# Kernel optimization log

Hardware: AMD Instinct MI355X
Metric: run time of the kernel (lower is better)

Reference implementation:

```python
import jax, jax.numpy as jnp
import numpy as np

EPS = 1e-5

def _conv1x1(x, w, b):
    # x: [B,C,H,W], w: [O,C], b: [O]
    return jnp.einsum('bchw,oc->bohw', x, w) + b[None, :, None, None]

def setup_inputs() -> dict:
    key = jax.random.key(0)
    ks = jax.random.split(key, 6)
    B, C, H, W = 8, 512, 64, 64
    Ck, Cv, Co = 256, 256, 512
    x = jax.random.normal(ks[0], (B, C, H, W), dtype=jnp.float32)
    Wk = jax.random.normal(ks[1], (Ck, C), dtype=jnp.float32) * 0.02
    bk = jnp.zeros((Ck,), dtype=jnp.float32)
    gamma = jnp.ones((Ck,), dtype=jnp.float32)
    beta = jnp.zeros((Ck,), dtype=jnp.float32)
    Wv = jax.random.normal(ks[2], (Cv, C), dtype=jnp.float32) * 0.02
    bv = jnp.zeros((Cv,), dtype=jnp.float32)
    Ww = jax.random.normal(ks[3], (Co, Cv), dtype=jnp.float32) * 0.02
    bw = jnp.zeros((Co,), dtype=jnp.float32)
    return {'x': x, 'Wk': Wk, 'bk': bk, 'gamma': gamma, 'beta': beta,
            'Wv': Wv, 'bv': bv, 'Ww': Ww, 'bw': bw}

def reference(x, Wk, bk, gamma, beta, Wv, bv, Ww, bw):
    B, C, H, W = x.shape
    # f_key == f_query (shared module): conv1x1 -> BN (training stats) -> ReLU
    qk = _conv1x1(x, Wk, bk)                      # [B,Ck,H,W]
    mean = qk.mean(axis=(0, 2, 3))
    var = qk.var(axis=(0, 2, 3))                  # biased variance, as torch BN training
    feat = jax.nn.relu((qk - mean[None, :, None, None])
                       * jax.lax.rsqrt(var + EPS)[None, :, None, None]
                       * gamma[None, :, None, None] + beta[None, :, None, None])
    value = _conv1x1(x, Wv, bv)                   # [B,Cv,H,W]
    Ck = feat.shape[1]
    Cv = value.shape[1]
    N = H * W
    q = feat.reshape(B, Ck, N).transpose(0, 2, 1)  # [B,N,Ck]
    k = feat.reshape(B, Ck, N)                     # [B,Ck,N]
    v = value.reshape(B, Cv, N).transpose(0, 2, 1) # [B,N,Cv]
    scale = Ck ** (-0.5)
    sim = jax.nn.softmax(jnp.matmul(q, k) * scale, axis=-1)  # [B,N,N]
    ctx = jnp.matmul(sim, v)                       # [B,N,Cv]
    ctx = ctx.transpose(0, 2, 1).reshape(B, Cv, H, W)
    out = _conv1x1(ctx, Ww, bw)                    # [B,Co,H,W]
    # scale==1 -> visualize_* upsamples are identity; sim_map visual is None
    return (out, feat, feat, value)
```

## Files before the change

### kernel.cpp

```cpp
#include <hip/hip_runtime.h>
#include <math.h>

constexpr int  Bn  = 8;
constexpr int  Cin = 512;
constexpr int  Nn  = 4096;
constexpr int  Ck  = 256;
constexpr int  Cv  = 256;
constexpr int  Co  = 512;

constexpr size_t F1_OFF  = (size_t)Bn * Co * Nn;
constexpr size_t F2_OFF  = F1_OFF + (size_t)Bn * Ck * Nn;
constexpr size_t VAL_OFF = F2_OFF + (size_t)Bn * Ck * Nn;

typedef __attribute__((ext_vector_type(8)))  short  short8;
typedef __attribute__((ext_vector_type(16))) float  f32x16;
typedef __attribute__((ext_vector_type(8)))  ushort ushort8;

static __device__ __forceinline__ ushort f2bf(float f) {
    union { float f; unsigned u; } x; x.f = f;
    unsigned r = x.u + 0x7fffu + ((x.u >> 16) & 1u);
    return (ushort)(r >> 16);
}

static __device__ __forceinline__ void gll16(const void* g, void* l) {
    __builtin_amdgcn_global_load_lds(
        (const __attribute__((address_space(1))) void*)g,
        (__attribute__((address_space(3))) void*)l, 16, 0, 0);
}

__global__ __launch_bounds__(256) void cast_w(const float* __restrict__ a,
                                              const float* __restrict__ b,
                                              const float* __restrict__ c,
                                              ushort* __restrict__ da,
                                              ushort* __restrict__ db,
                                              ushort* __restrict__ dc)
{
    const int tid   = blockIdx.x * 256 + threadIdx.x;
    const int which = tid >> 14;
    const int off   = (tid & 16383) * 8;
    const float* s = (which == 0) ? a : (which == 1) ? b : c;
    ushort*      d = (which == 0) ? da : (which == 1) ? db : dc;
    const float4 u = *(const float4*)(s + off);
    const float4 v = *(const float4*)(s + off + 4);
    ushort8 o;
    o[0] = f2bf(u.x); o[1] = f2bf(u.y); o[2] = f2bf(u.z); o[3] = f2bf(u.w);
    o[4] = f2bf(v.x); o[5] = f2bf(v.y); o[6] = f2bf(v.z); o[7] = f2bf(v.w);
    *(ushort8*)(d + off) = o;
}

__global__ __launch_bounds__(256) void transpose_c(const float* __restrict__ src,
                                                   ushort* __restrict__ dst, int C)
{
    const int b  = blockIdx.z;
    const int c0 = blockIdx.y * 64;
    const int n0 = blockIdx.x * 64;
    const int t  = threadIdx.x;
    __shared__ float T[64][65];
#pragma unroll
    for (int p = 0; p < 16; ++p) {
        const int flat = p * 256 + t;
        const int cc = flat >> 6, nn = flat & 63;
        T[cc][nn] = src[((size_t)b * C + c0 + cc) * Nn + n0 + nn];
    }
    __syncthreads();
#pragma unroll
    for (int p = 0; p < 16; ++p) {
        const int flat = p * 256 + t;
        const int nn = flat >> 6, cc = flat & 63;
        dst[((size_t)b * Nn + n0 + nn) * C + c0 + cc] = f2bf(T[cc][nn]);
    }
}

template <int K, bool DUAL>
__global__ __launch_bounds__(256) void gemm_bf(const ushort* __restrict__ XT,
                                               const ushort* __restrict__ Wb,
                                               const float*  __restrict__ bias,
                                               float* __restrict__ out,
                                               ushort* __restrict__ out_bf,
                                               int M)
{
    const int b  = blockIdx.z;
    const int m0 = blockIdx.y * 128;
    const int n0 = blockIdx.x * 128;
    const int t  = threadIdx.x;
    const int w  = t >> 6, L = t & 63;
    const int l31 = L & 31, hl = L >> 5;
    const int wm = (w >> 1) * 64, wn = (w & 1) * 64;

    __shared__ __align__(16) short As[128][72];
    __shared__ __align__(16) short Bs[128][72];

    const ushort* Xb = XT + (size_t)b * Nn * K;

    f32x16 acc[2][2];
#pragma unroll
    for (int a = 0; a < 2; ++a)
#pragma unroll
        for (int bb = 0; bb < 2; ++bb)
#pragma unroll
            for (int r = 0; r < 16; ++r) acc[a][bb][r] = 0.f;

    for (int k0 = 0; k0 < K; k0 += 64) {
        __syncthreads();
#pragma unroll
        for (int p = 0; p < 4; ++p) {
            const int e   = p * 256 + t;
            const int row = e >> 3, ko = (e & 7) * 8;
            *(short8*)&As[row][ko] =
                *(const short8*)(Wb + (size_t)(m0 + row) * K + k0 + ko);
            *(short8*)&Bs[row][ko] =
                *(const short8*)(Xb + (size_t)(n0 + row) * K + k0 + ko);
        }
        __syncthreads();
#pragma unroll
        for (int kc = 0; kc < 4; ++kc) {
            short8 Af[2], Bf[2];
#pragma unroll
            for (int a = 0; a < 2; ++a)
                Af[a] = *(const short8*)&As[wm + a * 32 + l31][kc * 16 + hl * 8];
#pragma unroll
            for (int bb = 0; bb < 2; ++bb)
                Bf[bb] = *(const short8*)&Bs[wn + bb * 32 + l31][kc * 16 + hl * 8];
#pragma unroll
            for (int a = 0; a < 2; ++a)
#pragma unroll
                for (int bb = 0; bb < 2; ++bb)
                    acc[a][bb] = __builtin_amdgcn_mfma_f32_32x32x16_bf16(
                        Af[a], Bf[bb], acc[a][bb], 0, 0, 0);
        }
    }

#pragma unroll
    for (int a = 0; a < 2; ++a)
#pragma unroll
        for (int r = 0; r < 16; ++r) {
            const int row = (r & 3) + 8 * (r >> 2) + 4 * hl;
            const int o   = m0 + wm + a * 32 + row;
            const float bv = bias[o];
            const size_t base = ((size_t)b * M + o) * Nn + n0 + wn + l31;
#pragma unroll
            for (int bb = 0; bb < 2; ++bb) {
                const float vv = acc[a][bb][r] + bv;
                out[base + bb * 32] = vv;
                if (DUAL) out_bf[base + bb * 32] = f2bf(vv);
            }
        }
}

__global__ __launch_bounds__(256) void bn_stats(const float* __restrict__ qk,
                                                const float* __restrict__ gamma,
                                                const float* __restrict__ beta,
                                                float* __restrict__ ss)
{
    const int o = blockIdx.x;
    const int t = threadIdx.x;
    float s = 0.f, sq = 0.f;
    for (int b = 0; b < Bn; ++b) {
        const float* p = qk + ((size_t)b * Ck + o) * Nn;
        for (int n = t * 4; n < Nn; n += 1024) {
            const float4 v = *(const float4*)(p + n);
            s  += v.x + v.y + v.z + v.w;
            sq += v.x * v.x + v.y * v.y + v.z * v.z + v.w * v.w;
        }
    }
    __shared__ float rs[256], rq[256];
    rs[t] = s; rq[t] = sq;
    __syncthreads();
    for (int off = 128; off > 0; off >>= 1) {
        if (t < off) { rs[t] += rs[t + off]; rq[t] += rq[t + off]; }
        __syncthreads();
    }
    if (t == 0) {
        const float cnt  = (float)(Bn * Nn);
        const float mean = rs[0] / cnt;
        const float var  = rq[0] / cnt - mean * mean;
        const float inv  = rsqrtf(var + 1e-5f);
        const float sc   = gamma[o] * inv;
        ss[o]       = sc;
        ss[256 + o] = beta[o] - mean * sc;
    }
}

__global__ __launch_bounds__(256) void bn_relu(const float* __restrict__ qk,
                                               const float* __restrict__ ss,
                                               float* __restrict__ f1,
                                               float* __restrict__ f2)
{
    const size_t tid = (size_t)blockIdx.x * 256 + threadIdx.x;
    const size_t idx = tid * 4;
    const int o = (int)((idx >> 12) & 255);
    const float sc = ss[o], sh = ss[256 + o];
    const float4 v = *(const float4*)(qk + idx);
    float4 r;
    r.x = fmaxf(v.x * sc + sh, 0.f);
    r.y = fmaxf(v.y * sc + sh, 0.f);
    r.z = fmaxf(v.z * sc + sh, 0.f);
    r.w = fmaxf(v.w * sc + sh, 0.f);
    *(float4*)(f1 + idx) = r;
    *(float4*)(f2 + idx) = r;
}

constexpr int LDS_BYTES = 148480;

__global__ __launch_bounds__(512) void attn_mfma(const ushort* __restrict__ featT,
                                                 const ushort* __restrict__ valB,
                                                 ushort* __restrict__ ctx)
{
    extern __shared__ __align__(16) char lds[];
    char* ldsK = lds;
    char* ldsV = lds + 65536;
    char* ldsP = lds + 131072;
    float* Lr  = (float*)(lds + 147456);

    const int b   = blockIdx.x;
    const int i0  = blockIdx.y * 128;
    const int t   = threadIdx.x;
    const int w   = t >> 6;
    const int L   = t & 63;
    const int l31 = L & 31, hl = L >> 5;
    const int ig  = w >> 1;
    const int ch  = w & 1;
    const int jsel = ch * 32;

    const int rbK = hl * 16 + (((jsel + l31) << 4) & 511);
    const int rotV = (l31 << 4) & 127;

    const ushort* F = featT + (size_t)b * Nn * Ck;
    const ushort* V = valB  + (size_t)b * Cv * Nn;
    const char*   Vg = (const char*)V;

    constexpr float CEXP = 0.09016844005556021f;
    constexpr int NT = Nn / 64;

#define STAGE(J0, BUF) do {                                                    \
        const char* Kg_ = (const char*)(F + (size_t)(J0) * Ck);                \
        char* Kd_ = ldsK + (BUF) * 32768;                                      \
        char* Vd_ = ldsV + (BUF) * 32768;                                      \
        _Pragma("unroll")                                                      \
        for (int p_ = 0; p_ < 4; ++p_) {                                       \
            const int c_ = w * 4 + p_;                                         \
            const int o_ = c_ * 1024 + L * 16;                                 \
            const int rK_ = o_ >> 9;                                           \
            gll16(Kg_ + rK_ * 512 + ((o_ - rK_ * 16) & 511), Kd_ + c_ * 1024); \
            const int rV_ = o_ >> 7;                                           \
            gll16(Vg + (size_t)rV_ * (Nn * 2) + (size_t)(J0) * 2               \
                     + ((o_ - rV_ * 16) & 127), Vd_ + c_ * 1024);              \
        }                                                                      \
    } while (0)

    STAGE(0, 0);

    short8 Qf[16];
    {
        const ushort* qp = F + ((size_t)(i0 + ig * 32 + l31)) * Ck + hl * 8;
#pragma unroll
        for (int kc = 0; kc < 16; ++kc)
            Qf[kc] = *(const short8*)(qp + kc * 16);
    }

    STAGE(64, 1);

    f32x16 Oacc[4];
#pragma unroll
    for (int c = 0; c < 4; ++c)
#pragma unroll
        for (int r = 0; r < 16; ++r) Oacc[c][r] = 0.f;
    float lsum = 0.f;

    int cur = 0;
    for (int jt = 0; jt < NT; ++jt) {
        if (jt < NT - 1) { asm volatile("s_waitcnt vmcnt(8)" ::: "memory"); }
        else             { asm volatile("s_waitcnt vmcnt(0)" ::: "memory"); }
        __builtin_amdgcn_s_barrier();

        const char* Kr = ldsK + cur * 32768 + (jsel + l31) * 512;

        f32x16 Sa, Sb;
#pragma unroll
        for (int r = 0; r < 16; ++r) { Sa[r] = 0.f; Sb[r] = 0.f; }
        __builtin_amdgcn_s_setprio(1);
#pragma unroll
        for (int kc = 0; kc < 8; ++kc) {
            const short8 K0 = *(const short8*)(Kr + ((kc * 64      + rbK) & 511));
            const short8 K1 = *(const short8*)(Kr + ((kc * 64 + 32 + rbK) & 511));
            Sa = __builtin_amdgcn_mfma_f32_32x32x16_bf16(K0, Qf[2 * kc],     Sa, 0, 0, 0);
            Sb = __builtin_amdgcn_mfma_f32_32x32x16_bf16(K1, Qf[2 * kc + 1], Sb, 0, 0, 0);
        }
        __builtin_amdgcn_s_setprio(0);

        unsigned pw[8];
#pragma unroll
        for (int r2 = 0; r2 < 8; ++r2) {
            const float p0 = exp2f((Sa[2 * r2]     + Sb[2 * r2])     * CEXP);
            const float p1 = exp2f((Sa[2 * r2 + 1] + Sb[2 * r2 + 1]) * CEXP);
            const unsigned u0 = (unsigned)f2bf(p0);
            const unsigned u1 = (unsigned)f2bf(p1);
            lsum += __uint_as_float(u0 << 16) + __uint_as_float(u1 << 16);
            pw[r2] = u0 | (u1 << 16);
        }
        {
            char* Pw = ldsP + ((ig * 4 + ch * 2) * 2 + hl) * 512 + l31 * 16;
#pragma unroll
            for (int g = 0; g < 2; ++g) {
                auto s02 = __builtin_amdgcn_permlane32_swap(pw[4 * g + 0], pw[4 * g + 2],
                                                            false, false);
                auto s13 = __builtin_amdgcn_permlane32_swap(pw[4 * g + 1], pw[4 * g + 3],
                                                            false, false);
                union { unsigned u[4]; short8 s; } pu;
                pu.u[0] = s02[0]; pu.u[1] = s13[0]; pu.u[2] = s02[1]; pu.u[3] = s13[1];
                *(short8*)(Pw + g * 1024) = pu.s;
            }
        }
        asm volatile("s_waitcnt lgkmcnt(0)" ::: "memory");
        __builtin_amdgcn_s_barrier();

        {
            const char* Pr  = ldsP + (ig * 8 + hl) * 512 + l31 * 16;
            const char* Vr2 = ldsV + cur * 32768 + (ch * 128 + l31) * 128;
            __builtin_amdgcn_s_setprio(1);
#pragma unroll
            for (int jb = 0; jb < 4; ++jb) {
                const short8 Pa = *(const short8*)(Pr + jb * 1024);
                const int jbyte = jb * 32 + hl * 16;
#pragma unroll
                for (int cvt = 0; cvt < 4; ++cvt) {
                    const short8 Vf = *(const short8*)(Vr2 + cvt * 4096
                                         + ((jbyte + rotV) & 127));
                    Oacc[cvt] = __builtin_amdgcn_mfma_f32_32x32x16_bf16(
                        Pa, Vf, Oacc[cvt], 0, 0, 0);
                }
            }
            __builtin_amdgcn_s_setprio(0);
        }

        asm volatile("s_waitcnt lgkmcnt(0)" ::: "memory");
        __builtin_amdgcn_s_barrier();
        if (jt + 2 < NT) { STAGE((size_t)(jt + 2) * 64, cur); }
        cur ^= 1;
    }
#undef STAGE

    {
        unsigned a = __float_as_uint(lsum), bcopy = a;
        auto sw = __builtin_amdgcn_permlane32_swap(a, bcopy, false, false);
        lsum = __uint_as_float(sw[0]) + __uint_as_float(sw[1]);
    }
    Lr[(ig * 2 + ch) * 32 + l31] = lsum;
    asm volatile("s_waitcnt lgkmcnt(0)" ::: "memory");
    __builtin_amdgcn_s_barrier();

    ushort* Cb = ctx + ((size_t)b * Nn + i0 + ig * 32) * Cv + ch * 128;
#pragma unroll
    for (int r = 0; r < 16; ++r) {
        const int row = (r & 3) + 8 * (r >> 2) + 4 * hl;
        const float lt = Lr[(ig * 2) * 32 + row] + Lr[(ig * 2 + 1) * 32 + row];
        const float linv = 1.f / lt;
        ushort* cp = Cb + (size_t)row * Cv + l31;
#pragma unroll
        for (int c4 = 0; c4 < 4; ++c4)
            cp[c4 * 32] = f2bf(Oacc[c4][r] * linv);
    }
}

extern "C" void kernel_launch(void* const* d_in, const int* in_sizes, int n_in,
                              void* d_out, int out_size, void* d_ws, size_t ws_size,
                              hipStream_t stream)
{
    const float* x     = (const float*)d_in[0];
    const float* Wk    = (const float*)d_in[1];
    const float* bk    = (const float*)d_in[2];
    const float* gamma = (const float*)d_in[3];
    const float* beta  = (const float*)d_in[4];
    const float* Wv    = (const float*)d_in[5];
    const float* bv    = (const float*)d_in[6];
    const float* Ww    = (const float*)d_in[7];
    const float* bw    = (const float*)d_in[8];

    float* out = (float*)d_out;
    float* f1  = out + F1_OFF;
    float* f2  = out + F2_OFF;
    float* val = out + VAL_OFF;

    ushort* xT    = (ushort*)d_ws;
    ushort* featT = xT;
    ushort* ctxb  = xT + (size_t)8388608;
    ushort* valB  = xT + (size_t)16777216;
    ushort* Wkb   = valB + (size_t)8388608;
    ushort* Wvb   = Wkb + 131072;
    ushort* Wwb   = Wvb + 131072;
    float*  ss    = (float*)(Wwb + 131072);

    static bool attn_attr_set = false;
    if (!attn_attr_set) {
        (void)hipFuncSetAttribute((const void*)attn_mfma,
                                  hipFuncAttributeMaxDynamicSharedMemorySize,
                                  LDS_BYTES);
        attn_attr_set = true;
    }

    cast_w<<<192, 256, 0, stream>>>(Wk, Wv, Ww, Wkb, Wvb, Wwb);
    transpose_c<<<dim3(Nn / 64, Cin / 64, Bn), 256, 0, stream>>>(x, xT, Cin);
    gemm_bf<512, false><<<dim3(Nn / 128, Ck / 128, Bn), 256, 0, stream>>>(
        xT, Wkb, bk, f1, nullptr, Ck);
    gemm_bf<512, true><<<dim3(Nn / 128, Cv / 128, Bn), 256, 0, stream>>>(
        xT, Wvb, bv, val, valB, Cv);
    bn_stats<<<Ck, 256, 0, stream>>>(f1, gamma, beta, ss);
    bn_relu<<<(Bn * Ck * Nn) / (256 * 4), 256, 0, stream>>>(f1, ss, f1, f2);
    transpose_c<<<dim3(Nn / 64, Ck / 64, Bn), 256, 0, stream>>>(f1, featT, Ck);
    attn_mfma<<<dim3(Bn, Nn / 128), 512, LDS_BYTES, stream>>>(featT, valB, ctxb);
    gemm_bf<256, false><<<dim3(Nn / 128, Co / 128, Bn), 256, 0, stream>>>(
        ctxb, Wwb, bw, out, nullptr, Co);
}
```

Baseline: 465.6 us.

## Software-pipeline attention so PV of previous tile overlaps QK of current

Restructures the attention loop so that each iteration computes QK^T for the current key tile while running the P·V MFMAs for the previous tile. It double-buffers the P tile in LDS and keeps this wave's own P fragment in registers, leaving one barrier per iteration instead of two. K is staged one tile ahead and V is loaded for the current tile, so V loads overlap the QK work. The transpose kernel is also vectorised to float4 loads and 16-byte bf16 stores. In exchange, LDS use grows to 160 KB, register pressure rises, and the loop waits with vmcnt(0) at every iteration.

```diff
diff --git a/kernel.cpp b/kernel.cpp
--- a/kernel.cpp
+++ b/kernel.cpp
@@ -57,17 +57,23 @@
     const int t  = threadIdx.x;
     __shared__ float T[64][65];
 #pragma unroll
-    for (int p = 0; p < 16; ++p) {
+    for (int p = 0; p < 4; ++p) {
         const int flat = p * 256 + t;
-        const int cc = flat >> 6, nn = flat & 63;
-        T[cc][nn] = src[((size_t)b * C + c0 + cc) * Nn + n0 + nn];
+        const int cc = flat >> 4, nn4 = (flat & 15) * 4;
+        const float4 v = *(const float4*)(
+            src + ((size_t)b * C + c0 + cc) * Nn + n0 + nn4);
+        T[cc][nn4]     = v.x; T[cc][nn4 + 1] = v.y;
+        T[cc][nn4 + 2] = v.z; T[cc][nn4 + 3] = v.w;
     }
     __syncthreads();
 #pragma unroll
-    for (int p = 0; p < 16; ++p) {
+    for (int p = 0; p < 2; ++p) {
         const int flat = p * 256 + t;
-        const int nn = flat >> 6, cc = flat & 63;
-        dst[((size_t)b * Nn + n0 + nn) * C + c0 + cc] = f2bf(T[cc][nn]);
+        const int nn = flat >> 3, cc0 = (flat & 7) * 8;
+        ushort8 o;
+#pragma unroll
+        for (int i = 0; i < 8; ++i) o[i] = f2bf(T[cc0 + i][nn]);
+        *(ushort8*)(dst + ((size_t)b * Nn + n0 + nn) * C + c0 + cc0) = o;
     }
 }
 
@@ -200,7 +206,7 @@
     *(float4*)(f2 + idx) = r;
 }
 
-constexpr int LDS_BYTES = 148480;
+constexpr int LDS_BYTES = 163840;
 
 __global__ __launch_bounds__(512) void attn_mfma(const ushort* __restrict__ featT,
                                                  const ushort* __restrict__ valB,
@@ -210,7 +216,6 @@
     char* ldsK = lds;
     char* ldsV = lds + 65536;
     char* ldsP = lds + 131072;
-    float* Lr  = (float*)(lds + 147456);
 
     const int b   = blockIdx.x;
     const int i0  = blockIdx.y * 128;
@@ -222,7 +227,7 @@
     const int ch  = w & 1;
     const int jsel = ch * 32;
 
-    const int rbK = hl * 16 + (((jsel + l31) << 4) & 511);
+    const int rbK  = hl * 16 + (((jsel + l31) << 4) & 511);
     const int rotV = (l31 << 4) & 127;
 
     const ushort* F = featT + (size_t)b * Nn * Ck;
@@ -232,24 +237,31 @@
     constexpr float CEXP = 0.09016844005556021f;
     constexpr int NT = Nn / 64;
 
-#define STAGE(J0, BUF) do {                                                    \
+#define STAGE_K(J0, BUF) do {                                                  \
         const char* Kg_ = (const char*)(F + (size_t)(J0) * Ck);                \
         char* Kd_ = ldsK + (BUF) * 32768;                                      \
-        char* Vd_ = ldsV + (BUF) * 32768;                                      \
         _Pragma("unroll")                                                      \
         for (int p_ = 0; p_ < 4; ++p_) {                                       \
             const int c_ = w * 4 + p_;                                         \
             const int o_ = c_ * 1024 + L * 16;                                 \
             const int rK_ = o_ >> 9;                                           \
             gll16(Kg_ + rK_ * 512 + ((o_ - rK_ * 16) & 511), Kd_ + c_ * 1024); \
+        }                                                                      \
+    } while (0)
+
+#define STAGE_V(J0, BUF) do {                                                  \
+        char* Vd_ = ldsV + (BUF) * 32768;                                      \
+        _Pragma("unroll")                                                      \
+        for (int p_ = 0; p_ < 4; ++p_) {                                       \
+            const int c_ = w * 4 + p_;                                         \
+            const int o_ = c_ * 1024 + L * 16;                                 \
             const int rV_ = o_ >> 7;                                           \
             gll16(Vg + (size_t)rV_ * (Nn * 2) + (size_t)(J0) * 2               \
                      + ((o_ - rV_ * 16) & 127), Vd_ + c_ * 1024);              \
         }                                                                      \
     } while (0)
 
-    STAGE(0, 0);
-
+    STAGE_K(0, 0);
     short8 Qf[16];
     {
         const ushort* qp = F + ((size_t)(i0 + ig * 32 + l31)) * Ck + hl * 8;
@@ -257,8 +269,8 @@
         for (int kc = 0; kc < 16; ++kc)
             Qf[kc] = *(const short8*)(qp + kc * 16);
     }
-
-    STAGE(64, 1);
+    asm volatile("s_waitcnt vmcnt(0)" ::: "memory");
+    __builtin_amdgcn_s_barrier();
 
     f32x16 Oacc[4];
 #pragma unroll
@@ -266,15 +278,15 @@
 #pragma unroll
         for (int r = 0; r < 16; ++r) Oacc[c][r] = 0.f;
     float lsum = 0.f;
+    short8 PfA{}, PfB{};
 
     int cur = 0;
-    for (int jt = 0; jt < NT; ++jt) {
-        if (jt < NT - 1) { asm volatile("s_waitcnt vmcnt(8)" ::: "memory"); }
-        else             { asm volatile("s_waitcnt vmcnt(0)" ::: "memory"); }
-        __builtin_amdgcn_s_barrier();
+    for (int s = 0; s < NT; ++s) {
+        const int jn = (s + 1 < NT ? s + 1 : NT - 1) * 64;
+        STAGE_K(jn, cur ^ 1);
+        STAGE_V((size_t)s * 64, cur);
 
         const char* Kr = ldsK + cur * 32768 + (jsel + l31) * 512;
-
         f32x16 Sa, Sb;
 #pragma unroll
         for (int r = 0; r < 16; ++r) { Sa[r] = 0.f; Sb[r] = 0.f; }
@@ -287,6 +299,40 @@
             Sb = __builtin_amdgcn_mfma_f32_32x32x16_bf16(K1, Qf[2 * kc + 1], Sb, 0, 0, 0);
         }
         __builtin_amdgcn_s_setprio(0);
+
+        if (s > 0) {
+            const char* Vr2 = ldsV + (cur ^ 1) * 32768 + (ch * 128 + l31) * 128;
+            const char* Pr  = ldsP + (cur ^ 1) * 16384
+                              + ((ig * 4 + (ch ^ 1) * 2) * 2 + hl) * 512 + l31 * 16;
+            const short8 Po0 = *(const short8*)(Pr);
+            const short8 Po1 = *(const short8*)(Pr + 1024);
+            __builtin_amdgcn_s_setprio(1);
+#pragma unroll
+            for (int g = 0; g < 2; ++g) {
+                const short8 Pa = g ? PfB : PfA;
+                const int jbyte = (ch * 2 + g) * 32 + hl * 16;
+#pragma unroll
+                for (int cvt = 0; cvt < 4; ++cvt) {
+                    const short8 Vf = *(const short8*)(Vr2 + cvt * 4096
+                                         + ((jbyte + rotV) & 127));
+                    Oacc[cvt] = __builtin_amdgcn_mfma_f32_32x32x16_bf16(
+                        Pa, Vf, Oacc[cvt], 0, 0, 0);
+                }
+            }
+#pragma unroll
+            for (int g = 0; g < 2; ++g) {
+                const short8 Pa = g ? Po1 : Po0;
+                const int jbyte = ((ch ^ 1) * 2 + g) * 32 + hl * 16;
+#pragma unroll
+                for (int cvt = 0; cvt < 4; ++cvt) {
+                    const short8 Vf = *(const short8*)(Vr2 + cvt * 4096
+                                         + ((jbyte + rotV) & 127));
+                    Oacc[cvt] = __builtin_amdgcn_mfma_f32_32x32x16_bf16(
+                        Pa, Vf, Oacc[cvt], 0, 0, 0);
+                }
+            }
+            __builtin_amdgcn_s_setprio(0);
+        }
 
         unsigned pw[8];
 #pragma unroll
@@ -299,7 +345,9 @@
             pw[r2] = u0 | (u1 << 16);
         }
         {
-            char* Pw = ldsP + ((ig * 4 + ch * 2) * 2 + hl) * 512 + l31 * 16;
+            char* Pw = ldsP + cur * 16384
+                       + ((ig * 4 + ch * 2) * 2 + hl) * 512 + l31 * 16;
+            short8 nf[2];
 #pragma unroll
             for (int g = 0; g < 2; ++g) {
                 auto s02 = __builtin_amdgcn_permlane32_swap(pw[4 * g + 0], pw[4 * g + 2],
@@ -308,43 +356,57 @@
                                                             false, false);
                 union { unsigned u[4]; short8 s; } pu;
                 pu.u[0] = s02[0]; pu.u[1] = s13[0]; pu.u[2] = s02[1]; pu.u[3] = s13[1];
+                nf[g] = pu.s;
                 *(short8*)(Pw + g * 1024) = pu.s;
             }
-        }
-        asm volatile("s_waitcnt lgkmcnt(0)" ::: "memory");
+            PfA = nf[0]; PfB = nf[1];
+        }
+
+        asm volatile("s_waitcnt vmcnt(0) lgkmcnt(0)" ::: "memory");
         __builtin_amdgcn_s_barrier();
-
-        {
-            const char* Pr  = ldsP + (ig * 8 + hl) * 512 + l31 * 16;
-            const char* Vr2 = ldsV + cur * 32768 + (ch * 128 + l31) * 128;
-            __builtin_amdgcn_s_setprio(1);
-#pragma unroll
-            for (int jb = 0; jb < 4; ++jb) {
-                const short8 Pa = *(const short8*)(Pr + jb * 1024);
-                const int jbyte = jb * 32 + hl * 16;
-#pragma unroll
-                for (int cvt = 0; cvt < 4; ++cvt) {
-                    const short8 Vf = *(const short8*)(Vr2 + cvt * 4096
-                                         + ((jbyte + rotV) & 127));
-                    Oacc[cvt] = __builtin_amdgcn_mfma_f32_32x32x16_bf16(
-                        Pa, Vf, Oacc[cvt], 0, 0, 0);
-                }
-            }
-            __builtin_amdgcn_s_setprio(0);
-        }
-
-        asm volatile("s_waitcnt lgkmcnt(0)" ::: "memory");
-        __builtin_amdgcn_s_barrier();
-        if (jt + 2 < NT) { STAGE((size_t)(jt + 2) * 64, cur); }
         cur ^= 1;
     }
-#undef STAGE
+#undef STAGE_K
+#undef STAGE_V
+
+    {
+        const char* Vr2 = ldsV + (cur ^ 1) * 32768 + (ch * 128 + l31) * 128;
+        const char* Pr  = ldsP + (cur ^ 1) * 16384
+                          + ((ig * 4 + (ch ^ 1) * 2) * 2 + hl) * 512 + l31 * 16;
+        const short8 Po0 = *(const short8*)(Pr);
+        const short8 Po1 = *(const short8*)(Pr + 1024);
+#pragma unroll
+        for (int g = 0; g < 2; ++g) {
+            const short8 Pa = g ? PfB : PfA;
+            const int jbyte = (ch * 2 + g) * 32 + hl * 16;
+#pragma unroll
+            for (int cvt = 0; cvt < 4; ++cvt) {
+                const short8 Vf = *(const short8*)(Vr2 + cvt * 4096
+                                     + ((jbyte + rotV) & 127));
+                Oacc[cvt] = __builtin_amdgcn_mfma_f32_32x32x16_bf16(
+                    Pa, Vf, Oacc[cvt], 0, 0, 0);
+            }
+        }
+#pragma unroll
+        for (int g = 0; g < 2; ++g) {
+            const short8 Pa = g ? Po1 : Po0;
+            const int jbyte = ((ch ^ 1) * 2 + g) * 32 + hl * 16;
+#pragma unroll
+            for (int cvt = 0; cvt < 4; ++cvt) {
+                const short8 Vf = *(const short8*)(Vr2 + cvt * 4096
+                                     + ((jbyte + rotV) & 127));
+                Oacc[cvt] = __builtin_amdgcn_mfma_f32_32x32x16_bf16(
+                    Pa, Vf, Oacc[cvt], 0, 0, 0);
+            }
+        }
+    }
 
     {
         unsigned a = __float_as_uint(lsum), bcopy = a;
         auto sw = __builtin_amdgcn_permlane32_swap(a, bcopy, false, false);
         lsum = __uint_as_float(sw[0]) + __uint_as_float(sw[1]);
     }
+    float* Lr = (float*)ldsP;
     Lr[(ig * 2 + ch) * 32 + l31] = lsum;
     asm volatile("s_waitcnt lgkmcnt(0)" ::: "memory");
     __builtin_amdgcn_s_barrier();
```

New measurement: 475.1 us. 2.0% more time.
